# Kernel tuning notes

Measured on AMD Instinct MI355X. Metric: run time of the kernel, lower is better.

## Reference

```python
import jax, jax.numpy as jnp
import numpy as np

N, K, D, H = 20000, 32, 256, 8
HD = D // H
DFF = 4 * D
EPS = 1e-5


def _layernorm(x, gamma, beta):
    mu = jnp.mean(x, axis=-1, keepdims=True)
    var = jnp.mean(jnp.square(x - mu), axis=-1, keepdims=True)
    return (x - mu) * jax.lax.rsqrt(var + EPS) * gamma + beta


def setup_inputs() -> dict:
    key = jax.random.key(0)
    ks = jax.random.split(key, 16)
    s = 0.02
    return {
        "x": jax.random.normal(ks[0], (N, D), jnp.float32),
        "attention_samples": jax.random.randint(ks[1], (N, K), 0, N),
        "Wq": jax.random.normal(ks[2], (D, D), jnp.float32) * s,
        "bq": jnp.zeros((D,), jnp.float32),
        "Wk": jax.random.normal(ks[3], (D, D), jnp.float32) * s,
        "bk": jnp.zeros((D,), jnp.float32),
        "Wv": jax.random.normal(ks[4], (D, D), jnp.float32) * s,
        "bv": jnp.zeros((D,), jnp.float32),
        "Wo": jax.random.normal(ks[5], (D, D), jnp.float32) * s,
        "bo": jnp.zeros((D,), jnp.float32),
        "W1": jax.random.normal(ks[6], (D, DFF), jnp.float32) * s,
        "b1": jnp.zeros((DFF,), jnp.float32),
        "W2": jax.random.normal(ks[7], (DFF, D), jnp.float32) * s,
        "b2": jnp.zeros((D,), jnp.float32),
        "g1": jnp.ones((D,), jnp.float32),
        "be1": jnp.zeros((D,), jnp.float32),
        "g2": jnp.ones((D,), jnp.float32),
        "be2": jnp.zeros((D,), jnp.float32),
    }


def reference(x, attention_samples, Wq, bq, Wk, bk, Wv, bv, Wo, bo,
              W1, b1, W2, b2, g1, be1, g2, be2):
    # --- per-node MHA: query = node itself, keys/values = k sampled neighbors ---
    q = (x @ Wq + bq).reshape(N, H, HD)                    # [N,H,hd]
    g = x[attention_samples]                               # [N,K,D] gathered neighbors
    kk = (g @ Wk + bk).reshape(N, K, H, HD)                # [N,K,H,hd]
    vv = (g @ Wv + bv).reshape(N, K, H, HD)
    scale = 1.0 / jnp.sqrt(jnp.asarray(HD, x.dtype))
    scores = jnp.einsum("nhd,nkhd->nhk", q, kk) * scale    # [N,H,K]
    attn = jax.nn.softmax(scores, axis=-1)
    o = jnp.einsum("nhk,nkhd->nhd", attn, vv).reshape(N, D)
    attn_out = o @ Wo + bo                                 # out_proj
    x = _layernorm(x + attn_out, g1, be1)
    # --- FFN ---
    ff = jax.nn.relu(x @ W1 + b1) @ W2 + b2
    x = _layernorm(x + ff, g2, be2)
    return x
```

## Files before the change

kernel.cpp:

```cpp
#include <hip/hip_runtime.h>

#define NN 20000
#define KNEI 32
#define DIM 256
#define NHEAD 8
#define HDIM 32
#define DFFN 1024
#define QKVD 768

typedef __attribute__((ext_vector_type(8))) __bf16 bf16x8;
typedef __attribute__((ext_vector_type(8))) unsigned short u16x8;
typedef __attribute__((ext_vector_type(4))) unsigned short u16x4;
typedef __attribute__((ext_vector_type(4))) float f32x4;
typedef __attribute__((ext_vector_type(2))) float f32x2;

static __device__ __forceinline__ float b2f(unsigned short u) {
    return __builtin_bit_cast(float, (unsigned)u << 16);
}
static __device__ __forceinline__ float blo(unsigned w) {
    return __builtin_bit_cast(float, w << 16);
}
static __device__ __forceinline__ float bhi(unsigned w) {
    return __builtin_bit_cast(float, w & 0xffff0000u);
}
static __device__ __forceinline__ unsigned short f2b(float f) {
    unsigned u = __builtin_bit_cast(unsigned, f);
    return (unsigned short)((u + 0x7fff + ((u >> 16) & 1)) >> 16);
}

static __device__ __forceinline__ unsigned char fp8enc(float v) {
#if defined(__HIP_DEVICE_COMPILE__) && __has_builtin(__builtin_amdgcn_cvt_pk_fp8_f32)
    return (unsigned char)(__builtin_amdgcn_cvt_pk_fp8_f32(v, v, 0u, false) & 0xffu);
#else
    unsigned u = __builtin_bit_cast(unsigned, v);
    unsigned s = u >> 31;
    unsigned a = u & 0x7fffffffu;
    if (a >= 0x43e00000u) return (unsigned char)((s << 7) | 0x7e);
    float af = __builtin_bit_cast(float, a);
    if (af < 0.015625f) {
        unsigned r = (unsigned)(af * 512.0f + 0.5f);
        if (r >= 8u) return (unsigned char)((s << 7) | 0x08);
        return (unsigned char)((s << 7) | r);
    }
    unsigned lsb = (a >> 20) & 1u;
    a += 0x7ffffu + lsb;
    unsigned e = (a >> 23) - 120u;
    unsigned m = (a >> 20) & 7u;
    unsigned code = (e << 3) | m;
    if (code > 0x7eu) code = 0x7eu;
    return (unsigned char)((s << 7) | code);
#endif
}

template<int SEL>
static __device__ __forceinline__ float fp8dec(unsigned word) {
#if defined(__HIP_DEVICE_COMPILE__) && __has_builtin(__builtin_amdgcn_cvt_f32_fp8)
    return __builtin_amdgcn_cvt_f32_fp8(word, SEL);
#else
    unsigned b = (word >> (SEL * 8)) & 0xffu;
    unsigned s = (b >> 7) & 1u;
    unsigned e = (b >> 3) & 0xfu;
    unsigned m = b & 7u;
    float v;
    if (e == 0) v = (float)m * 0.001953125f;
    else        v = __builtin_bit_cast(float, ((e + 120u) << 23) | (m << 20));
    return s ? -v : v;
#endif
}

template<bool HI>
static __device__ __forceinline__ f32x2 fp8pk(unsigned word) {
#if defined(__HIP_DEVICE_COMPILE__) && __has_builtin(__builtin_amdgcn_cvt_pk_f32_fp8)
    return __builtin_amdgcn_cvt_pk_f32_fp8((int)word, HI);
#else
    f32x2 r;
    r.x = fp8dec<HI ? 2 : 0>(word);
    r.y = fp8dec<HI ? 3 : 1>(word);
    return r;
#endif
}

#define GLD16(src, dst)                                                          \
    __builtin_amdgcn_global_load_lds(                                            \
        (const __attribute__((address_space(1))) void*)(const void*)(src),       \
        (__attribute__((address_space(3))) void*)(void*)(dst), 16, 0, 0)

template<int BM, int RELU, int WF32, int WBF16, int SPLIT>
__global__ __launch_bounds__(256) void gemm_mfma(const unsigned short* __restrict__ A,
                                                 const unsigned short* __restrict__ Bt,
                                                 const float* __restrict__ bias,
                                                 float* __restrict__ Cf,
                                                 unsigned short* __restrict__ Cb,
                                                 unsigned char* __restrict__ kvp,
                                                 int M, int N, int K)
{
    constexpr int BN = 128, BK = 32;
    constexpr int MI = BM / 32;
    constexpr int NI = BN / 32;

    __shared__ unsigned short As[BM * BK];
    __shared__ unsigned short Bs[BN * BK];

    const int tid  = threadIdx.x;
    const int wid  = tid >> 6;
    const int lane = tid & 63;
    const int bm = blockIdx.x * BM;
    const int bn = blockIdx.y * BN;
    const int wr = (wid >> 1) * (BM / 2);
    const int wc = (wid & 1) * (BN / 2);
    const int r0   = lane & 15;
    const int kblk = (lane >> 4) * 8;

    f32x4 acc[MI][NI];
    #pragma unroll
    for (int i = 0; i < MI; ++i)
        #pragma unroll
        for (int j = 0; j < NI; ++j)
            acc[i][j] = (f32x4){0.f, 0.f, 0.f, 0.f};

    for (int k0 = 0; k0 < K; k0 += BK) {
        #pragma unroll
        for (int t = 0; t < (BM * 4) / 256; ++t) {
            int c = t * 256 + tid;
            int row = bm + (c >> 2);
            if (row >= M) row = M - 1;
            GLD16(A + (size_t)row * K + k0 + (c & 3) * 8,
                  &As[(t * 256 + wid * 64) * 8]);
        }
        #pragma unroll
        for (int t = 0; t < (BN * 4) / 256; ++t) {
            int c = t * 256 + tid;
            GLD16(Bt + (size_t)(bn + (c >> 2)) * K + k0 + (c & 3) * 8,
                  &Bs[(t * 256 + wid * 64) * 8]);
        }
        __syncthreads();

        bf16x8 af[MI], bfr[NI];
        #pragma unroll
        for (int mi = 0; mi < MI; ++mi)
            af[mi] = __builtin_bit_cast(bf16x8,
                     *(const u16x8*)&As[(wr + mi * 16 + r0) * BK + kblk]);
        #pragma unroll
        for (int ni = 0; ni < NI; ++ni)
            bfr[ni] = __builtin_bit_cast(bf16x8,
                     *(const u16x8*)&Bs[(wc + ni * 16 + r0) * BK + kblk]);
        #pragma unroll
        for (int mi = 0; mi < MI; ++mi)
            #pragma unroll
            for (int ni = 0; ni < NI; ++ni)
                acc[mi][ni] = __builtin_amdgcn_mfma_f32_16x16x32_bf16(
                    af[mi], bfr[ni], acc[mi][ni], 0, 0, 0);
        __syncthreads();
    }

    const int r4 = (lane >> 4) * 4;
    #pragma unroll
    for (int mi = 0; mi < MI; ++mi)
        #pragma unroll
        for (int ni = 0; ni < NI; ++ni) {
            const int col = bn + wc + ni * 16 + r0;
            const float bb = bias[col];
            #pragma unroll
            for (int r = 0; r < 4; ++r) {
                const int row = bm + wr + mi * 16 + r4 + r;
                if (row < M) {
                    float v = acc[mi][ni][r] + bb;
                    if (RELU) v = fmaxf(v, 0.f);
                    if (SPLIT) {
                        if (col < 256) {
                            Cb[(size_t)row * DIM + col] = f2b(v);
                        } else {
                            const int cc  = col - 256;
                            const int isV = cc >> 8;
                            const int hh  = (cc & 255) >> 5;
                            const int dd  = cc & 31;
                            kvp[((size_t)(hh >> 1) * NN + row) * 128
                                + isV * 64 + (hh & 1) * 32 + dd] = fp8enc(v);
                        }
                    } else {
                        if (WF32)  Cf[(size_t)row * N + col] = v;
                        if (WBF16) Cb[(size_t)row * N + col] = f2b(v);
                    }
                }
            }
        }
}

__global__ __launch_bounds__(256) void attn_f8(const unsigned short* __restrict__ q,
                                               const unsigned char* __restrict__ kvp,
                                               const int* __restrict__ samp,
                                               unsigned short* __restrict__ o)
{
    const int bid = blockIdx.x;
    const int hp  = bid & 3;
    const int tid = threadIdx.x;
    const int wid = tid >> 6;
    const int n   = (bid >> 2) * 4 + wid;
    const int lane = tid & 63;
    const int j = lane & 31;
    const int hs = lane >> 5;
    const int h = hp * 2 + hs;

    const int kidx = samp[n * KNEI + j];

    const uint4* qp = (const uint4*)(q + (size_t)n * DIM + h * HDIM);
    const uint4 qa = qp[0], qb = qp[1], qc = qp[2], qd = qp[3];
    const unsigned qw[16] = {qa.x, qa.y, qa.z, qa.w, qb.x, qb.y, qb.z, qb.w,
                             qc.x, qc.y, qc.z, qc.w, qd.x, qd.y, qd.z, qd.w};

    const unsigned char* krow = kvp + ((size_t)hp * NN + kidx) * 128 + hs * 32;
    const uint4 k0 = *(const uint4*)krow;
    const uint4 k1 = *(const uint4*)(krow + 16);
    const unsigned kw[8] = {k0.x, k0.y, k0.z, k0.w, k1.x, k1.y, k1.z, k1.w};

    float s = 0.f;
    #pragma unroll
    for (int i = 0; i < 8; ++i) {
        f32x2 ka = fp8pk<false>(kw[i]);
        f32x2 kb = fp8pk<true>(kw[i]);
        unsigned q0 = qw[2 * i], q1 = qw[2 * i + 1];
        s = fmaf(blo(q0), ka.x, s);
        s = fmaf(bhi(q0), ka.y, s);
        s = fmaf(blo(q1), kb.x, s);
        s = fmaf(bhi(q1), kb.y, s);
    }
    s *= 0.17677669529663687f;

    float m = s;
    #pragma unroll
    for (int sh = 16; sh; sh >>= 1) m = fmaxf(m, __shfl_xor(m, sh));
    float e = __expf(s - m);
    float sum = e;
    #pragma unroll
    for (int sh = 16; sh; sh >>= 1) sum += __shfl_xor(sum, sh);
    const float p = __fdividef(e, sum);

    const int d = j;
    const int pbits = __builtin_bit_cast(int, p);
    const int pbase = hs * 128;
    const unsigned vbase = (unsigned)((size_t)hp * NN * 128) + 64 + hs * 32 + d;
    float acc = 0.f;
    #pragma unroll
    for (int jj = 0; jj < KNEI; ++jj) {
        const int kj = __builtin_amdgcn_readlane(kidx, jj);
        const float pj = __builtin_bit_cast(float,
            __builtin_amdgcn_ds_bpermute(pbase + jj * 4, pbits));
        acc = fmaf(pj, fp8dec<0>((unsigned)kvp[vbase + (unsigned)kj * 128u]), acc);
    }
    o[(size_t)n * DIM + h * HDIM + d] = f2b(acc);
}

template<int XF32, int WFOUT>
__global__ __launch_bounds__(256) void add_ln(const float* __restrict__ xf,
                                              const unsigned short* __restrict__ xb,
                                              const unsigned short* __restrict__ y,
                                              const float* __restrict__ gamma,
                                              const float* __restrict__ beta,
                                              float* __restrict__ outf,
                                              unsigned short* __restrict__ outb, int M)
{
    const int row = blockIdx.x * 4 + (threadIdx.x >> 6);
    const int lane = threadIdx.x & 63;
    if (row >= M) return;

    float s0, s1, s2, s3;
    if (XF32) {
        const float4 xv = *(const float4*)(xf + (size_t)row * DIM + lane * 4);
        s0 = xv.x; s1 = xv.y; s2 = xv.z; s3 = xv.w;
    } else {
        const u16x4 xv = *(const u16x4*)(xb + (size_t)row * DIM + lane * 4);
        s0 = b2f(xv[0]); s1 = b2f(xv[1]); s2 = b2f(xv[2]); s3 = b2f(xv[3]);
    }
    const u16x4 yv = *(const u16x4*)(y + (size_t)row * DIM + lane * 4);
    s0 += b2f(yv[0]); s1 += b2f(yv[1]); s2 += b2f(yv[2]); s3 += b2f(yv[3]);

    float sum = s0 + s1 + s2 + s3;
    float sq = s0 * s0 + s1 * s1 + s2 * s2 + s3 * s3;
    #pragma unroll
    for (int sh = 32; sh; sh >>= 1) {
        sum += __shfl_xor(sum, sh);
        sq  += __shfl_xor(sq, sh);
    }
    float mean = sum * (1.f / 256.f);
    float var = sq * (1.f / 256.f) - mean * mean;
    float rstd = rsqrtf(var + 1e-5f);

    const float4 gv = *(const float4*)(gamma + lane * 4);
    const float4 bv = *(const float4*)(beta + lane * 4);
    float o0 = (s0 - mean) * rstd * gv.x + bv.x;
    float o1 = (s1 - mean) * rstd * gv.y + bv.y;
    float o2 = (s2 - mean) * rstd * gv.z + bv.z;
    float o3 = (s3 - mean) * rstd * gv.w + bv.w;
    if (WFOUT) {
        float4 ov = { o0, o1, o2, o3 };
        *(float4*)(outf + (size_t)row * DIM + lane * 4) = ov;
    } else {
        u16x4 bb = { f2b(o0), f2b(o1), f2b(o2), f2b(o3) };
        *(u16x4*)(outb + (size_t)row * DIM + lane * 4) = bb;
    }
}

__global__ __launch_bounds__(256) void cvt_bf16(const float* __restrict__ in,
                                                unsigned short* __restrict__ out, int n4)
{
    int i = blockIdx.x * 256 + threadIdx.x;
    if (i < n4) {
        float4 v = ((const float4*)in)[i];
        u16x4 b = { f2b(v.x), f2b(v.y), f2b(v.z), f2b(v.w) };
        ((u16x4*)out)[i] = b;
    }
}

__global__ __launch_bounds__(256) void cvt_transpose(const float* __restrict__ W,
                                                     unsigned short* __restrict__ Wt,
                                                     int K, int N)
{
    __shared__ float t[32][33];
    const int n0 = blockIdx.x * 32, k0 = blockIdx.y * 32;
    const int tx = threadIdx.x & 31, ty = threadIdx.x >> 5;
    #pragma unroll
    for (int i = 0; i < 32; i += 8)
        t[ty + i][tx] = W[(size_t)(k0 + ty + i) * N + n0 + tx];
    __syncthreads();
    #pragma unroll
    for (int i = 0; i < 32; i += 8)
        Wt[(size_t)(n0 + ty + i) * K + k0 + tx] = f2b(t[tx][ty + i]);
}

__global__ __launch_bounds__(256) void cvt_transpose4(const float* __restrict__ Wa,
                                                      const float* __restrict__ Wb,
                                                      const float* __restrict__ Wc,
                                                      const float* __restrict__ Wd,
                                                      unsigned short* __restrict__ Ta,
                                                      unsigned short* __restrict__ Tb,
                                                      unsigned short* __restrict__ Tc,
                                                      unsigned short* __restrict__ Td)
{
    const float* W; unsigned short* T;
    switch (blockIdx.z) {
        case 0:  W = Wa; T = Ta; break;
        case 1:  W = Wb; T = Tb; break;
        case 2:  W = Wc; T = Tc; break;
        default: W = Wd; T = Td; break;
    }
    __shared__ float t[32][33];
    const int n0 = blockIdx.x * 32, k0 = blockIdx.y * 32;
    const int tx = threadIdx.x & 31, ty = threadIdx.x >> 5;
    #pragma unroll
    for (int i = 0; i < 32; i += 8)
        t[ty + i][tx] = W[(size_t)(k0 + ty + i) * DIM + n0 + tx];
    __syncthreads();
    #pragma unroll
    for (int i = 0; i < 32; i += 8)
        T[(size_t)(n0 + ty + i) * DIM + k0 + tx] = f2b(t[tx][ty + i]);
}

__global__ void concat_bias(const float* a, const float* b, const float* c, float* out)
{
    int i = blockIdx.x * 256 + threadIdx.x;
    if (i < 256) out[i] = a[i];
    else if (i < 512) out[i] = b[i - 256];
    else if (i < 768) out[i] = c[i - 512];
}

extern "C" void kernel_launch(void* const* d_in, const int* in_sizes, int n_in,
                              void* d_out, int out_size, void* d_ws, size_t ws_size,
                              hipStream_t stream)
{
    const float* x    = (const float*)d_in[0];
    const int*   samp = (const int*)  d_in[1];
    const float* Wq = (const float*)d_in[2];  const float* bq = (const float*)d_in[3];
    const float* Wk = (const float*)d_in[4];  const float* bk = (const float*)d_in[5];
    const float* Wv = (const float*)d_in[6];  const float* bv = (const float*)d_in[7];
    const float* Wo = (const float*)d_in[8];  const float* bo = (const float*)d_in[9];
    const float* W1 = (const float*)d_in[10]; const float* b1 = (const float*)d_in[11];
    const float* W2 = (const float*)d_in[12]; const float* b2 = (const float*)d_in[13];
    const float* g1 = (const float*)d_in[14]; const float* be1 = (const float*)d_in[15];
    const float* g2 = (const float*)d_in[16]; const float* be2 = (const float*)d_in[17];
    float* out = (float*)d_out;

    char* w = (char*)d_ws;
    const size_t MB = 1u << 20;
    unsigned short* WqkvT = (unsigned short*)(w + 0);
    unsigned short* WoT   = (unsigned short*)(w + 393216);
    unsigned short* W1T   = (unsigned short*)(w + 524288);
    unsigned short* W2T   = (unsigned short*)(w + 1048576);
    float*          bqkv  = (float*)(w + 1572864);
    unsigned short* xb    = (unsigned short*)(w + 2 * MB);
    unsigned short* qb    = (unsigned short*)(w + 13 * MB);
    unsigned char*  kvp   = (unsigned char*) (w + 24 * MB);
    unsigned short* ob    = xb;
    unsigned short* attno = (unsigned short*)(w + 35 * MB);
    unsigned short* x1b   = (unsigned short*)(w + 46 * MB);
    unsigned short* hmid  = (unsigned short*)(w + 57 * MB);
    unsigned short* ffb   = attno;

    const dim3 blk(256);

    cvt_transpose4<<<dim3(8, 8, 4), blk, 0, stream>>>(
        Wq, Wk, Wv, Wo, WqkvT, WqkvT + 256 * 256, WqkvT + 512 * 256, WoT);
    cvt_transpose<<<dim3(32, 8), blk, 0, stream>>>(W1, W1T, DIM, DFFN);
    cvt_transpose<<<dim3(8, 32), blk, 0, stream>>>(W2, W2T, DFFN, DIM);
    concat_bias<<<dim3(3), blk, 0, stream>>>(bq, bk, bv, bqkv);
    cvt_bf16<<<dim3((NN * DIM / 4 + 255) / 256), blk, 0, stream>>>(x, xb, NN * DIM / 4);

    gemm_mfma<128, 0, 0, 0, 1><<<dim3(157, 6), blk, 0, stream>>>(
        xb, WqkvT, bqkv, nullptr, qb, kvp, NN, QKVD, DIM);

    attn_f8<<<dim3(NN), blk, 0, stream>>>(qb, kvp, samp, ob);

    gemm_mfma<64, 0, 0, 1, 0><<<dim3(313, 2), blk, 0, stream>>>(
        ob, WoT, bo, nullptr, attno, nullptr, NN, DIM, DIM);
    add_ln<1, 0><<<dim3(NN / 4), blk, 0, stream>>>(x, nullptr, attno, g1, be1,
                                                   nullptr, x1b, NN);

    gemm_mfma<128, 1, 0, 1, 0><<<dim3(157, 8), blk, 0, stream>>>(
        x1b, W1T, b1, nullptr, hmid, nullptr, NN, DFFN, DIM);
    gemm_mfma<64, 0, 0, 1, 0><<<dim3(313, 2), blk, 0, stream>>>(
        hmid, W2T, b2, nullptr, ffb, nullptr, NN, DIM, DFFN);
    add_ln<0, 1><<<dim3(NN / 4), blk, 0, stream>>>(nullptr, x1b, ffb, g2, be2,
                                                   out, nullptr, NN);
}
```

Before: 190.7 us.

## Vectorize attention V gather via LDS and fuse prep kernels into one launch

The attention PV loop now stages each wave's softmax probabilities and neighbor row offsets in shared memory. Each lane loads 4 fp8 V values with one 32-bit load over 8 neighbors, instead of a byte load per neighbor across all 32, and partial sums are then reduced across lane groups with shuffles. This cuts the number of gather load instructions and the bpermute traffic, at the cost of the extra shuffle reductions. Separately, the five weight-transpose, bias-concat and x-conversion kernels are merged into a single launch to reduce launch overhead.

Measured after the change: 171.0 us. 1.11x faster.

```diff
diff --git a/kernel.cpp b/kernel.cpp
--- a/kernel.cpp
+++ b/kernel.cpp
@@ -191,6 +191,8 @@
                                                const int* __restrict__ samp,
                                                unsigned short* __restrict__ o)
 {
+    __shared__ int pkbuf[4][128];
+
     const int bid = blockIdx.x;
     const int hp  = bid & 3;
     const int tid = threadIdx.x;
@@ -235,19 +237,33 @@
     for (int sh = 16; sh; sh >>= 1) sum += __shfl_xor(sum, sh);
     const float p = __fdividef(e, sum);
 
-    const int d = j;
-    const int pbits = __builtin_bit_cast(int, p);
-    const int pbase = hs * 128;
-    const unsigned vbase = (unsigned)((size_t)hp * NN * 128) + 64 + hs * 32 + d;
-    float acc = 0.f;
-    #pragma unroll
-    for (int jj = 0; jj < KNEI; ++jj) {
-        const int kj = __builtin_amdgcn_readlane(kidx, jj);
-        const float pj = __builtin_bit_cast(float,
-            __builtin_amdgcn_ds_bpermute(pbase + jj * 4, pbits));
-        acc = fmaf(pj, fp8dec<0>((unsigned)kvp[vbase + (unsigned)kj * 128u]), acc);
-    }
-    o[(size_t)n * DIM + h * HDIM + d] = f2b(acc);
+    pkbuf[wid][hs * 64 + j * 2]     = __builtin_bit_cast(int, p);
+    pkbuf[wid][hs * 64 + j * 2 + 1] = kidx << 7;
+
+    const int jg = j >> 3, d8 = j & 7;
+    const unsigned vconst = (unsigned)((size_t)hp * NN) * 128u + 64u + hs * 32 + d8 * 4;
+    float a0 = 0.f, a1 = 0.f, a2 = 0.f, a3 = 0.f;
+    #pragma unroll
+    for (int jj = 0; jj < 8; ++jj) {
+        const int jn = jg * 8 + jj;
+        const int2 pk = *(const int2*)&pkbuf[wid][hs * 64 + jn * 2];
+        const float pj = __builtin_bit_cast(float, pk.x);
+        const unsigned vw = *(const unsigned*)(kvp + vconst + (unsigned)pk.y);
+        f32x2 vlo = fp8pk<false>(vw);
+        f32x2 vhi = fp8pk<true>(vw);
+        a0 = fmaf(pj, vlo.x, a0);
+        a1 = fmaf(pj, vlo.y, a1);
+        a2 = fmaf(pj, vhi.x, a2);
+        a3 = fmaf(pj, vhi.y, a3);
+    }
+    a0 += __shfl_xor(a0, 8);  a1 += __shfl_xor(a1, 8);
+    a2 += __shfl_xor(a2, 8);  a3 += __shfl_xor(a3, 8);
+    a0 += __shfl_xor(a0, 16); a1 += __shfl_xor(a1, 16);
+    a2 += __shfl_xor(a2, 16); a3 += __shfl_xor(a3, 16);
+    if (jg == 0) {
+        u16x4 ov = { f2b(a0), f2b(a1), f2b(a2), f2b(a3) };
+        *(u16x4*)(o + (size_t)n * DIM + h * HDIM + d8 * 4) = ov;
+    }
 }
 
 template<int XF32, int WFOUT>
@@ -300,67 +316,72 @@
     }
 }
 
-__global__ __launch_bounds__(256) void cvt_bf16(const float* __restrict__ in,
-                                                unsigned short* __restrict__ out, int n4)
-{
-    int i = blockIdx.x * 256 + threadIdx.x;
-    if (i < n4) {
-        float4 v = ((const float4*)in)[i];
-        u16x4 b = { f2b(v.x), f2b(v.y), f2b(v.z), f2b(v.w) };
-        ((u16x4*)out)[i] = b;
-    }
-}
-
-__global__ __launch_bounds__(256) void cvt_transpose(const float* __restrict__ W,
-                                                     unsigned short* __restrict__ Wt,
-                                                     int K, int N)
-{
-    __shared__ float t[32][33];
-    const int n0 = blockIdx.x * 32, k0 = blockIdx.y * 32;
-    const int tx = threadIdx.x & 31, ty = threadIdx.x >> 5;
+static __device__ __forceinline__ void trans_tile(const float* __restrict__ W,
+                                                  unsigned short* __restrict__ T,
+                                                  float (*sh)[33],
+                                                  int n0, int k0, int N, int K, int tidx)
+{
+    const int tx = tidx & 31, ty = tidx >> 5;
     #pragma unroll
     for (int i = 0; i < 32; i += 8)
-        t[ty + i][tx] = W[(size_t)(k0 + ty + i) * N + n0 + tx];
+        sh[ty + i][tx] = W[(size_t)(k0 + ty + i) * N + n0 + tx];
     __syncthreads();
     #pragma unroll
     for (int i = 0; i < 32; i += 8)
-        Wt[(size_t)(n0 + ty + i) * K + k0 + tx] = f2b(t[tx][ty + i]);
-}
-
-__global__ __launch_bounds__(256) void cvt_transpose4(const float* __restrict__ Wa,
-                                                      const float* __restrict__ Wb,
-                                                      const float* __restrict__ Wc,
-                                                      const float* __restrict__ Wd,
-                                                      unsigned short* __restrict__ Ta,
-                                                      unsigned short* __restrict__ Tb,
-                                                      unsigned short* __restrict__ Tc,
-                                                      unsigned short* __restrict__ Td)
-{
-    const float* W; unsigned short* T;
-    switch (blockIdx.z) {
-        case 0:  W = Wa; T = Ta; break;
-        case 1:  W = Wb; T = Tb; break;
-        case 2:  W = Wc; T = Tc; break;
-        default: W = Wd; T = Td; break;
-    }
-    __shared__ float t[32][33];
-    const int n0 = blockIdx.x * 32, k0 = blockIdx.y * 32;
-    const int tx = threadIdx.x & 31, ty = threadIdx.x >> 5;
-    #pragma unroll
-    for (int i = 0; i < 32; i += 8)
-        t[ty + i][tx] = W[(size_t)(k0 + ty + i) * DIM + n0 + tx];
-    __syncthreads();
-    #pragma unroll
-    for (int i = 0; i < 32; i += 8)
-        T[(size_t)(n0 + ty + i) * DIM + k0 + tx] = f2b(t[tx][ty + i]);
-}
-
-__global__ void concat_bias(const float* a, const float* b, const float* c, float* out)
-{
-    int i = blockIdx.x * 256 + threadIdx.x;
-    if (i < 256) out[i] = a[i];
-    else if (i < 512) out[i] = b[i - 256];
-    else if (i < 768) out[i] = c[i - 512];
+        T[(size_t)(n0 + ty + i) * K + k0 + tx] = f2b(sh[tx][ty + i]);
+}
+
+__global__ __launch_bounds__(256) void prep_all(const float* __restrict__ Wq,
+                                                const float* __restrict__ Wk,
+                                                const float* __restrict__ Wv,
+                                                const float* __restrict__ Wo,
+                                                const float* __restrict__ W1,
+                                                const float* __restrict__ W2,
+                                                const float* __restrict__ bq,
+                                                const float* __restrict__ bk,
+                                                const float* __restrict__ bv,
+                                                const float* __restrict__ x,
+                                                unsigned short* __restrict__ WqkvT,
+                                                unsigned short* __restrict__ WoT,
+                                                unsigned short* __restrict__ W1T,
+                                                unsigned short* __restrict__ W2T,
+                                                float* __restrict__ bqkv,
+                                                unsigned short* __restrict__ xb)
+{
+    __shared__ float sh[32][33];
+    const int bid = blockIdx.x;
+    const int tidx = threadIdx.x;
+
+    if (bid < 256) {
+        const float* W; unsigned short* T;
+        switch (bid >> 6) {
+            case 0:  W = Wq; T = WqkvT;           break;
+            case 1:  W = Wk; T = WqkvT + 65536;   break;
+            case 2:  W = Wv; T = WqkvT + 131072;  break;
+            default: W = Wo; T = WoT;             break;
+        }
+        const int t = bid & 63;
+        trans_tile(W, T, sh, (t & 7) * 32, (t >> 3) * 32, DIM, DIM, tidx);
+    } else if (bid < 512) {
+        const int t = bid - 256;
+        trans_tile(W1, W1T, sh, (t & 31) * 32, (t >> 5) * 32, DFFN, DIM, tidx);
+    } else if (bid < 768) {
+        const int t = bid - 512;
+        trans_tile(W2, W2T, sh, (t & 7) * 32, (t >> 3) * 32, DIM, DFFN, tidx);
+    } else if (bid == 768) {
+        if (tidx < 256) {
+            bqkv[tidx]       = bq[tidx];
+            bqkv[tidx + 256] = bk[tidx];
+            bqkv[tidx + 512] = bv[tidx];
+        }
+    } else {
+        const int i = (bid - 769) * 256 + tidx;
+        if (i < NN * DIM / 4) {
+            float4 v = ((const float4*)x)[i];
+            u16x4 b = { f2b(v.x), f2b(v.y), f2b(v.z), f2b(v.w) };
+            ((u16x4*)xb)[i] = b;
+        }
+    }
 }
 
 extern "C" void kernel_launch(void* const* d_in, const int* in_sizes, int n_in,
@@ -397,12 +418,9 @@
 
     const dim3 blk(256);
 
-    cvt_transpose4<<<dim3(8, 8, 4), blk, 0, stream>>>(
-        Wq, Wk, Wv, Wo, WqkvT, WqkvT + 256 * 256, WqkvT + 512 * 256, WoT);
-    cvt_transpose<<<dim3(32, 8), blk, 0, stream>>>(W1, W1T, DIM, DFFN);
-    cvt_transpose<<<dim3(8, 32), blk, 0, stream>>>(W2, W2T, DFFN, DIM);
-    concat_bias<<<dim3(3), blk, 0, stream>>>(bq, bk, bv, bqkv);
-    cvt_bf16<<<dim3((NN * DIM / 4 + 255) / 256), blk, 0, stream>>>(x, xb, NN * DIM / 4);
+    prep_all<<<dim3(769 + NN * DIM / 4 / 256), blk, 0, stream>>>(
+        Wq, Wk, Wv, Wo, W1, W2, bq, bk, bv, x,
+        WqkvT, WoT, W1T, W2T, bqkv, xb);
 
     gemm_mfma<128, 0, 0, 0, 1><<<dim3(157, 6), blk, 0, stream>>>(
         xb, WqkvT, bqkv, nullptr, qb, kvp, NN, QKVD, DIM);
```
